# Performance work log

Measured on AMD Instinct MI355X. Metric: run time of the kernel, lower is better.

Reference implementation:

```python
import jax, jax.numpy as jnp
import numpy as np

HIST_SIZE = 200
DIM = 64
HIDDEN = 32
NEG_INF = -2.0**32 + 1.0  # matches tf padding constant


def setup_inputs() -> dict:
    key = jax.random.key(0)
    k1, k2, k3, k4, k5 = jax.random.split(key, 5)
    B = 4096
    cand = jax.random.normal(k1, (B, DIM), dtype=jnp.float32)
    hist = jax.random.normal(k2, (B, HIST_SIZE, DIM), dtype=jnp.float32)
    hisLens = jax.random.randint(k3, (B,), 0, HIST_SIZE, dtype=jnp.int32)
    # Glorot-normal-ish params
    attW1 = jax.random.normal(k4, (4 * DIM, HIDDEN), dtype=jnp.float32) * (2.0 / (4 * DIM + HIDDEN)) ** 0.5
    attB1 = jnp.zeros((HIDDEN,), dtype=jnp.float32)
    attW2 = jax.random.normal(k5, (HIDDEN, 1), dtype=jnp.float32) * (2.0 / (HIDDEN + 1)) ** 0.5
    attB2 = jnp.zeros((1,), dtype=jnp.float32)
    return {"candidate_embedding": cand, "hist_embeddings": hist, "hisLens": hisLens,
            "attW1": attW1, "attB1": attB1, "attW2": attW2, "attB2": attB2}


def reference(candidate_embedding, hist_embeddings, hisLens, attW1, attB1, attW2, attB2):
    # candidate: [B, d] -> broadcast over hist steps [B, S, d]
    cand = candidate_embedding[:, None, :]
    # per-step feature concat: [cand, hist, cand*hist, cand-hist] -> [B, S, 4d]
    z3 = jnp.concatenate([
        jnp.broadcast_to(cand, hist_embeddings.shape),
        hist_embeddings,
        cand * hist_embeddings,
        cand - hist_embeddings,
    ], axis=-1)
    # tiny 2-layer MLP scorer -> [B, S]
    h = jax.nn.relu(jnp.einsum('bsf,fh->bsh', z3, attW1) + attB1)
    scores = (jnp.einsum('bsh,ho->bso', h, attW2) + attB2)[..., 0]
    # sequence mask then scale (same order as original), softmax over hist dim
    mask = jnp.arange(HIST_SIZE)[None, :] < hisLens[:, None]
    scores = jnp.where(mask, scores, NEG_INF) / (DIM ** 0.5)
    w = jax.nn.softmax(scores, axis=-1)  # [B, S]
    # weighted sum of history embeddings -> [B, d]
    return jnp.einsum('bs,bsd->bd', w, hist_embeddings)
```

## Files before the change

kernel.cpp:

```cpp
#include <hip/hip_runtime.h>
#include <math.h>

#define HS    200
#define DIMV  64
#define HID   32
#define NTH   256
#define NB    2

typedef __attribute__((ext_vector_type(8))) short short8;
typedef __attribute__((ext_vector_type(4))) float f32x4;
typedef __bf16 bf2_t __attribute__((ext_vector_type(2)));
typedef float  f2_t  __attribute__((ext_vector_type(2)));

__device__ __forceinline__ unsigned cvt2(float x, float y) {
    f2_t f = {x, y};
    bf2_t bv = __builtin_convertvector(f, bf2_t);
    union { bf2_t b; unsigned u; } un;
    un.b = bv;
    return un.u;
}

template<int CTRL>
__device__ __forceinline__ float dpp_add(float x) {
    int y = __builtin_amdgcn_update_dpp(0, __float_as_int(x), CTRL, 0xF, 0xF, true);
    return x + __int_as_float(y);
}
#define ROR1  0x121
#define ROR2  0x122
#define ROR4  0x124
#define ROR8  0x128
#define QXOR1 0xB1
#define QXOR2 0x4E
#define HMIRR 0x141
__device__ __forceinline__ float swz_xor16(float x) {
    return __int_as_float(__builtin_amdgcn_ds_swizzle(__float_as_int(x), 0x401F));
}
__device__ __forceinline__ float rfl(float x) {
    return __int_as_float(__builtin_amdgcn_readfirstlane(__float_as_int(x)));
}


__global__ __launch_bounds__(NTH, 4) void din_attn_kernel(
    const float* __restrict__ cand,
    const float* __restrict__ hist,
    const int*   __restrict__ lens,
    const float* __restrict__ W1,
    const float* __restrict__ B1,
    const float* __restrict__ W2,
    const float* __restrict__ B2,
    float* __restrict__ out)
{
    __shared__ __align__(16) unsigned short s_Mt[NB][HID * 64];
    __shared__ float s_c[NB][HID];
    __shared__ __align__(16) float s_comb[4][DIMV];
    __shared__ float s_m[4], s_l[4];

    const int tid  = threadIdx.x;
    const int lane = tid & 63, wid = tid >> 6;
    const int b0   = blockIdx.x * NB;

    {
        const int h = tid & 31, fg = tid >> 5;
        float wbd[8], wcc[8];
        #pragma unroll
        for (int ff = 0; ff < 8; ++ff) {
            int f = fg * 8 + ff;
            wbd[ff] = W1[(DIMV + f) * HID + h] - W1[(3 * DIMV + f) * HID + h];
            wcc[ff] = W1[(2 * DIMV + f) * HID + h];
        }
        #pragma unroll
        for (int k = 0; k < NB; ++k) {
            const float* cb = cand + (size_t)(b0 + k) * DIMV + fg * 8;
            float4 cA = *(const float4*)cb;
            float4 cB = *(const float4*)(cb + 4);
            float cf[8] = {cA.x, cA.y, cA.z, cA.w, cB.x, cB.y, cB.z, cB.w};
            float m[8];
            #pragma unroll
            for (int ff = 0; ff < 8; ++ff) m[ff] = fmaf(cf[ff], wcc[ff], wbd[ff]);
            uint4 mw = make_uint4(cvt2(m[0], m[1]), cvt2(m[2], m[3]),
                                  cvt2(m[4], m[5]), cvt2(m[6], m[7]));
            *(uint4*)&s_Mt[k][h * 64 + (fg ^ (h & 7)) * 8] = mw;
        }
        const int hc = tid >> 3, fgc = tid & 7;
        float wad[8];
        #pragma unroll
        for (int ff = 0; ff < 8; ++ff) {
            int f = fgc * 8 + ff;
            wad[ff] = W1[f * HID + hc] + W1[(3 * DIMV + f) * HID + hc];
        }
        float b1 = B1[hc];
        #pragma unroll
        for (int k = 0; k < NB; ++k) {
            const float* cb = cand + (size_t)(b0 + k) * DIMV + fgc * 8;
            float4 cA = *(const float4*)cb;
            float4 cB = *(const float4*)(cb + 4);
            float p = cA.x * wad[0] + cA.y * wad[1] + cA.z * wad[2] + cA.w * wad[3]
                    + cB.x * wad[4] + cB.y * wad[5] + cB.z * wad[6] + cB.w * wad[7];
            p = dpp_add<QXOR1>(p);
            p = dpp_add<QXOR2>(p);
            p = dpp_add<HMIRR>(p);
            if ((tid & 7) == 0) s_c[k][hc] = p + b1;
        }
    }
    __syncthreads();

    const int kb   = wid >> 1, hf = wid & 1;
    const int b    = b0 + kb;
    const int len  = lens[b];
    const bool uni = (len == 0);
    const int nrow  = uni ? HS : len;
    const int nhalf = (nrow + 1 - hf) >> 1;
    const int nt    = (nhalf + 15) >> 4;
    const int lc    = lane & 15, lg = lane >> 4;
    const float* hb = hist + (size_t)b * (HS * DIMV);

    short8 b00 = *(const short8*)&s_Mt[kb][lc * 64        + ((lg)     ^ (lc & 7)) * 8];
    short8 b01 = *(const short8*)&s_Mt[kb][lc * 64        + ((4 + lg) ^ (lc & 7)) * 8];
    short8 b10 = *(const short8*)&s_Mt[kb][(16 + lc) * 64 + ((lg)     ^ (lc & 7)) * 8];
    short8 b11 = *(const short8*)&s_Mt[kb][(16 + lc) * 64 + ((4 + lg) ^ (lc & 7)) * 8];
    const float c0  = s_c[kb][lc],     c1  = s_c[kb][16 + lc];
    const float w20 = W2[lc] * 0.125f, w21 = W2[16 + lc] * 0.125f;

    float m_run = -3.0e38f, l_acc = 0.f;
    float o0[8] = {0.f, 0.f, 0.f, 0.f, 0.f, 0.f, 0.f, 0.f};
    float o1[8] = {0.f, 0.f, 0.f, 0.f, 0.f, 0.f, 0.f, 0.f};

    for (int rt = 0; rt < nt; ++rt) {
        int i = rt * 16 + lc;
        if (i > nhalf - 1) i = nhalf - 1;
        const int s = 2 * i + hf;
        const float* ap = hb + s * 64 + lg * 8;
        float4 A00 = *(const float4*)ap;
        float4 A01 = *(const float4*)(ap + 4);
        float4 A10 = *(const float4*)(ap + 32);
        float4 A11 = *(const float4*)(ap + 36);
        union { uint4 u; short8 s8; } u0, u1;
        u0.u = make_uint4(cvt2(A00.x, A00.y), cvt2(A00.z, A00.w),
                          cvt2(A01.x, A01.y), cvt2(A01.z, A01.w));
        u1.u = make_uint4(cvt2(A10.x, A10.y), cvt2(A10.z, A10.w),
                          cvt2(A11.x, A11.y), cvt2(A11.z, A11.w));

        f32x4 acc0 = {c0, c0, c0, c0};
        acc0 = __builtin_amdgcn_mfma_f32_16x16x32_bf16(u0.s8, b00, acc0, 0, 0, 0);
        acc0 = __builtin_amdgcn_mfma_f32_16x16x32_bf16(u1.s8, b01, acc0, 0, 0, 0);
        f32x4 acc1 = {c1, c1, c1, c1};
        acc1 = __builtin_amdgcn_mfma_f32_16x16x32_bf16(u0.s8, b10, acc1, 0, 0, 0);
        acc1 = __builtin_amdgcn_mfma_f32_16x16x32_bf16(u1.s8, b11, acc1, 0, 0, 0);

        float p[4];
        #pragma unroll
        for (int r = 0; r < 4; ++r)
            p[r] = fmaxf(acc0[r], 0.f) * w20 + fmaxf(acc1[r], 0.f) * w21;
        #pragma unroll
        for (int r = 0; r < 4; ++r) {
            p[r] = dpp_add<ROR1>(p[r]);
            p[r] = dpp_add<ROR2>(p[r]);
            p[r] = dpp_add<ROR4>(p[r]);
            p[r] = dpp_add<ROR8>(p[r]);
        }
        #pragma unroll
        for (int r = 0; r < 4; ++r) {
            int row = rt * 16 + lg * 4 + r;
            p[r] = (row < nhalf) ? (uni ? 0.f : p[r]) : -4.0e9f;
        }
        float tmax = fmaxf(fmaxf(p[0], p[1]), fmaxf(p[2], p[3]));
        tmax = fmaxf(tmax, swz_xor16(tmax));
        tmax = fmaxf(tmax, __shfl_xor(tmax, 32));
        tmax = rfl(tmax);
        if (tmax > m_run + 8.f) {
            float sf = __expf(m_run - tmax);
            #pragma unroll
            for (int j = 0; j < 8; ++j) { o0[j] *= sf; o1[j] *= sf; }
            l_acc *= sf;
            m_run = tmax;
        }
        float e[4];
        #pragma unroll
        for (int r = 0; r < 4; ++r) e[r] = __expf(p[r] - m_run);
        l_acc += (e[0] + e[1]) + (e[2] + e[3]);

        float t0 = (lc & 1) ? e[1] : e[0];
        float t1 = (lc & 1) ? e[3] : e[2];
        float es = (lc & 2) ? t1 : t0;
        int   src = (((lc & 3) | ((lc >> 2) << 4)) << 2);
        float wrow = __int_as_float(
            __builtin_amdgcn_ds_bpermute(src, __float_as_int(es)));

        o0[0] = fmaf(wrow, A00.x, o0[0]); o0[1] = fmaf(wrow, A00.y, o0[1]);
        o0[2] = fmaf(wrow, A00.z, o0[2]); o0[3] = fmaf(wrow, A00.w, o0[3]);
        o0[4] = fmaf(wrow, A01.x, o0[4]); o0[5] = fmaf(wrow, A01.y, o0[5]);
        o0[6] = fmaf(wrow, A01.z, o0[6]); o0[7] = fmaf(wrow, A01.w, o0[7]);
        o1[0] = fmaf(wrow, A10.x, o1[0]); o1[1] = fmaf(wrow, A10.y, o1[1]);
        o1[2] = fmaf(wrow, A10.z, o1[2]); o1[3] = fmaf(wrow, A10.w, o1[3]);
        o1[4] = fmaf(wrow, A11.x, o1[4]); o1[5] = fmaf(wrow, A11.y, o1[5]);
        o1[6] = fmaf(wrow, A11.z, o1[6]); o1[7] = fmaf(wrow, A11.w, o1[7]);
    }

    l_acc += swz_xor16(l_acc);
    l_acc += __shfl_xor(l_acc, 32);
    #pragma unroll
    for (int j = 0; j < 8; ++j) {
        float x = o0[j];
        x = dpp_add<ROR1>(x); x = dpp_add<ROR2>(x);
        x = dpp_add<ROR4>(x); x = dpp_add<ROR8>(x);
        o0[j] = x;
        float y = o1[j];
        y = dpp_add<ROR1>(y); y = dpp_add<ROR2>(y);
        y = dpp_add<ROR4>(y); y = dpp_add<ROR8>(y);
        o1[j] = y;
    }
    if (lc == 0) {
        float* d = &s_comb[wid][lg * 8];
        *(float4*)d        = make_float4(o0[0], o0[1], o0[2], o0[3]);
        *(float4*)(d + 4)  = make_float4(o0[4], o0[5], o0[6], o0[7]);
        *(float4*)(d + 32) = make_float4(o1[0], o1[1], o1[2], o1[3]);
        *(float4*)(d + 36) = make_float4(o1[4], o1[5], o1[6], o1[7]);
        if (lane == 0) { s_m[wid] = m_run; s_l[wid] = l_acc; }
    }
    __syncthreads();

    if (wid < NB) {
        const int w0 = 2 * wid, w1 = 2 * wid + 1;
        const float m0 = s_m[w0], m1 = s_m[w1];
        const float M  = fmaxf(m0, m1);
        const float a0 = __expf(m0 - M), a1 = __expf(m1 - M);
        const float den = a0 * s_l[w0] + a1 * s_l[w1];
        const float o   = a0 * s_comb[w0][lane] + a1 * s_comb[w1][lane];
        out[(size_t)(b0 + wid) * DIMV + lane] = o / den;
    }
}

extern "C" void kernel_launch(void* const* d_in, const int* in_sizes, int n_in,
                              void* d_out, int out_size, void* d_ws, size_t ws_size,
                              hipStream_t stream) {
    const float* cand = (const float*)d_in[0];
    const float* hist = (const float*)d_in[1];
    const int*   lens = (const int*)d_in[2];
    const float* W1   = (const float*)d_in[3];
    const float* B1   = (const float*)d_in[4];
    const float* W2   = (const float*)d_in[5];
    const float* B2   = (const float*)d_in[6];
    float* out = (float*)d_out;

    const int B = in_sizes[0] / DIMV;
    const int GRID = B / NB;
    din_attn_kernel<<<GRID, NTH, 0, stream>>>(cand, hist, lens, W1, B1, W2, B2, out);
}
```

Baseline: 35.34 us.

## Balance history tiles across waves with an LDS work counter over four batches

```diff
diff --git a/kernel.cpp b/kernel.cpp
--- a/kernel.cpp
+++ b/kernel.cpp
@@ -5,7 +5,7 @@
 #define DIMV  64
 #define HID   32
 #define NTH   256
-#define NB    2
+#define NB    4
 
 typedef __attribute__((ext_vector_type(8))) short short8;
 typedef __attribute__((ext_vector_type(4))) float f32x4;
@@ -19,6 +19,8 @@
     un.b = bv;
     return un.u;
 }
+__device__ __forceinline__ float blo(unsigned u) { return __uint_as_float(u << 16); }
+__device__ __forceinline__ float bhi(unsigned u) { return __uint_as_float(u & 0xFFFF0000u); }
 
 template<int CTRL>
 __device__ __forceinline__ float dpp_add(float x) {
@@ -52,8 +54,9 @@
 {
     __shared__ __align__(16) unsigned short s_Mt[NB][HID * 64];
     __shared__ float s_c[NB][HID];
-    __shared__ __align__(16) float s_comb[4][DIMV];
-    __shared__ float s_m[4], s_l[4];
+    __shared__ __align__(16) float s_om[4][NB][DIMV];
+    __shared__ float s_mm[4][NB], s_ll[4][NB];
+    __shared__ int   s_ctr;
 
     const int tid  = threadIdx.x;
     const int lane = tid & 63, wid = tid >> 6;
@@ -101,35 +104,78 @@
             p = dpp_add<HMIRR>(p);
             if ((tid & 7) == 0) s_c[k][hc] = p + b1;
         }
+        if (tid < 16) { s_mm[tid >> 2][tid & 3] = -3.0e38f; s_ll[tid >> 2][tid & 3] = 0.f; }
+        if (tid == 0) s_ctr = 0;
     }
     __syncthreads();
 
-    const int kb   = wid >> 1, hf = wid & 1;
-    const int b    = b0 + kb;
-    const int len  = lens[b];
-    const bool uni = (len == 0);
-    const int nrow  = uni ? HS : len;
-    const int nhalf = (nrow + 1 - hf) >> 1;
-    const int nt    = (nhalf + 15) >> 4;
-    const int lc    = lane & 15, lg = lane >> 4;
-    const float* hb = hist + (size_t)b * (HS * DIMV);
-
-    short8 b00 = *(const short8*)&s_Mt[kb][lc * 64        + ((lg)     ^ (lc & 7)) * 8];
-    short8 b01 = *(const short8*)&s_Mt[kb][lc * 64        + ((4 + lg) ^ (lc & 7)) * 8];
-    short8 b10 = *(const short8*)&s_Mt[kb][(16 + lc) * 64 + ((lg)     ^ (lc & 7)) * 8];
-    short8 b11 = *(const short8*)&s_Mt[kb][(16 + lc) * 64 + ((4 + lg) ^ (lc & 7)) * 8];
-    const float c0  = s_c[kb][lc],     c1  = s_c[kb][16 + lc];
+    const int lc = lane & 15, lg = lane >> 4;
     const float w20 = W2[lc] * 0.125f, w21 = W2[16 + lc] * 0.125f;
-
+    const int len0 = lens[b0 + 0], len1 = lens[b0 + 1];
+    const int len2 = lens[b0 + 2], len3 = lens[b0 + 3];
+    const int nr0 = (len0 == 0) ? HS : len0, nr1 = (len1 == 0) ? HS : len1;
+    const int nr2 = (len2 == 0) ? HS : len2, nr3 = (len3 == 0) ? HS : len3;
+    const int t0 = (nr0 + 15) >> 4, t1 = (nr1 + 15) >> 4;
+    const int t2 = (nr2 + 15) >> 4, t3 = (nr3 + 15) >> 4;
+    const int q1 = t0, q2 = t0 + t1, q3 = t0 + t1 + t2;
+    const int total = q3 + t3;
+
+    int curk = -1, nrow = 0;
+    bool uni = false;
+    float c0 = 0.f, c1 = 0.f;
     float m_run = -3.0e38f, l_acc = 0.f;
     float o0[8] = {0.f, 0.f, 0.f, 0.f, 0.f, 0.f, 0.f, 0.f};
     float o1[8] = {0.f, 0.f, 0.f, 0.f, 0.f, 0.f, 0.f, 0.f};
-
-    for (int rt = 0; rt < nt; ++rt) {
+    const float* hb = hist;
+
+    auto FLUSH = [&](int kk) {
+        float l = l_acc;
+        l += swz_xor16(l);
+        l += __shfl_xor(l, 32);
+        #pragma unroll
+        for (int jj = 0; jj < 8; ++jj) {
+            float x = o0[jj];
+            x = dpp_add<ROR1>(x); x = dpp_add<ROR2>(x);
+            x = dpp_add<ROR4>(x); x = dpp_add<ROR8>(x);
+            o0[jj] = x;
+            float y = o1[jj];
+            y = dpp_add<ROR1>(y); y = dpp_add<ROR2>(y);
+            y = dpp_add<ROR4>(y); y = dpp_add<ROR8>(y);
+            o1[jj] = y;
+        }
+        if (lc == 0) {
+            float* d = &s_om[wid][kk][lg * 8];
+            *(float4*)d        = make_float4(o0[0], o0[1], o0[2], o0[3]);
+            *(float4*)(d + 4)  = make_float4(o0[4], o0[5], o0[6], o0[7]);
+            *(float4*)(d + 32) = make_float4(o1[0], o1[1], o1[2], o1[3]);
+            *(float4*)(d + 36) = make_float4(o1[4], o1[5], o1[6], o1[7]);
+            if (lane == 0) { s_mm[wid][kk] = m_run; s_ll[wid][kk] = l; }
+        }
+    };
+
+    for (;;) {
+        int j = 0;
+        if (lane == 0) j = atomicAdd(&s_ctr, 1);
+        j = __shfl(j, 0);
+        if (j >= total) break;
+        const int k  = (j >= q1) + (j >= q2) + (j >= q3);
+        const int rt = j - ((k == 0) ? 0 : (k == 1) ? q1 : (k == 2) ? q2 : q3);
+        if (k != curk) {
+            if (curk >= 0) FLUSH(curk);
+            curk = k;
+            m_run = -3.0e38f; l_acc = 0.f;
+            #pragma unroll
+            for (int jj = 0; jj < 8; ++jj) { o0[jj] = 0.f; o1[jj] = 0.f; }
+            c0 = s_c[k][lc]; c1 = s_c[k][16 + lc];
+            const int lk = (k == 0) ? len0 : (k == 1) ? len1 : (k == 2) ? len2 : len3;
+            uni  = (lk == 0);
+            nrow = (k == 0) ? nr0 : (k == 1) ? nr1 : (k == 2) ? nr2 : nr3;
+            hb   = hist + (size_t)(b0 + k) * (HS * DIMV);
+        }
+
         int i = rt * 16 + lc;
-        if (i > nhalf - 1) i = nhalf - 1;
-        const int s = 2 * i + hf;
-        const float* ap = hb + s * 64 + lg * 8;
+        if (i > nrow - 1) i = nrow - 1;
+        const float* ap = hb + i * 64 + lg * 8;
         float4 A00 = *(const float4*)ap;
         float4 A01 = *(const float4*)(ap + 4);
         float4 A10 = *(const float4*)(ap + 32);
@@ -140,6 +186,12 @@
         u1.u = make_uint4(cvt2(A10.x, A10.y), cvt2(A10.z, A10.w),
                           cvt2(A11.x, A11.y), cvt2(A11.z, A11.w));
 
+        const unsigned short* mt = s_Mt[k];
+        short8 b00 = *(const short8*)&mt[lc * 64        + ((lg)     ^ (lc & 7)) * 8];
+        short8 b01 = *(const short8*)&mt[lc * 64        + ((4 + lg) ^ (lc & 7)) * 8];
+        short8 b10 = *(const short8*)&mt[(16 + lc) * 64 + ((lg)     ^ (lc & 7)) * 8];
+        short8 b11 = *(const short8*)&mt[(16 + lc) * 64 + ((4 + lg) ^ (lc & 7)) * 8];
+
         f32x4 acc0 = {c0, c0, c0, c0};
         acc0 = __builtin_amdgcn_mfma_f32_16x16x32_bf16(u0.s8, b00, acc0, 0, 0, 0);
         acc0 = __builtin_amdgcn_mfma_f32_16x16x32_bf16(u1.s8, b01, acc0, 0, 0, 0);
@@ -161,7 +213,7 @@
         #pragma unroll
         for (int r = 0; r < 4; ++r) {
             int row = rt * 16 + lg * 4 + r;
-            p[r] = (row < nhalf) ? (uni ? 0.f : p[r]) : -4.0e9f;
+            p[r] = (row < nrow) ? (uni ? 0.f : p[r]) : -4.0e9f;
         }
         float tmax = fmaxf(fmaxf(p[0], p[1]), fmaxf(p[2], p[3]));
         tmax = fmaxf(tmax, swz_xor16(tmax));
@@ -170,7 +222,7 @@
         if (tmax > m_run + 8.f) {
             float sf = __expf(m_run - tmax);
             #pragma unroll
-            for (int j = 0; j < 8; ++j) { o0[j] *= sf; o1[j] *= sf; }
+            for (int jj = 0; jj < 8; ++jj) { o0[jj] *= sf; o1[jj] *= sf; }
             l_acc *= sf;
             m_run = tmax;
         }
@@ -179,53 +231,35 @@
         for (int r = 0; r < 4; ++r) e[r] = __expf(p[r] - m_run);
         l_acc += (e[0] + e[1]) + (e[2] + e[3]);
 
-        float t0 = (lc & 1) ? e[1] : e[0];
-        float t1 = (lc & 1) ? e[3] : e[2];
-        float es = (lc & 2) ? t1 : t0;
+        float s0 = (lc & 1) ? e[1] : e[0];
+        float s1 = (lc & 1) ? e[3] : e[2];
+        float es = (lc & 2) ? s1 : s0;
         int   src = (((lc & 3) | ((lc >> 2) << 4)) << 2);
         float wrow = __int_as_float(
             __builtin_amdgcn_ds_bpermute(src, __float_as_int(es)));
 
-        o0[0] = fmaf(wrow, A00.x, o0[0]); o0[1] = fmaf(wrow, A00.y, o0[1]);
-        o0[2] = fmaf(wrow, A00.z, o0[2]); o0[3] = fmaf(wrow, A00.w, o0[3]);
-        o0[4] = fmaf(wrow, A01.x, o0[4]); o0[5] = fmaf(wrow, A01.y, o0[5]);
-        o0[6] = fmaf(wrow, A01.z, o0[6]); o0[7] = fmaf(wrow, A01.w, o0[7]);
-        o1[0] = fmaf(wrow, A10.x, o1[0]); o1[1] = fmaf(wrow, A10.y, o1[1]);
-        o1[2] = fmaf(wrow, A10.z, o1[2]); o1[3] = fmaf(wrow, A10.w, o1[3]);
-        o1[4] = fmaf(wrow, A11.x, o1[4]); o1[5] = fmaf(wrow, A11.y, o1[5]);
-        o1[6] = fmaf(wrow, A11.z, o1[6]); o1[7] = fmaf(wrow, A11.w, o1[7]);
+        o0[0] = fmaf(wrow, blo(u0.u.x), o0[0]); o0[1] = fmaf(wrow, bhi(u0.u.x), o0[1]);
+        o0[2] = fmaf(wrow, blo(u0.u.y), o0[2]); o0[3] = fmaf(wrow, bhi(u0.u.y), o0[3]);
+        o0[4] = fmaf(wrow, blo(u0.u.z), o0[4]); o0[5] = fmaf(wrow, bhi(u0.u.z), o0[5]);
+        o0[6] = fmaf(wrow, blo(u0.u.w), o0[6]); o0[7] = fmaf(wrow, bhi(u0.u.w), o0[7]);
+        o1[0] = fmaf(wrow, blo(u1.u.x), o1[0]); o1[1] = fmaf(wrow, bhi(u1.u.x), o1[1]);
+        o1[2] = fmaf(wrow, blo(u1.u.y), o1[2]); o1[3] = fmaf(wrow, bhi(u1.u.y), o1[3]);
+        o1[4] = fmaf(wrow, blo(u1.u.z), o1[4]); o1[5] = fmaf(wrow, bhi(u1.u.z), o1[5]);
+        o1[6] = fmaf(wrow, blo(u1.u.w), o1[6]); o1[7] = fmaf(wrow, bhi(u1.u.w), o1[7]);
     }
-
-    l_acc += swz_xor16(l_acc);
-    l_acc += __shfl_xor(l_acc, 32);
-    #pragma unroll
-    for (int j = 0; j < 8; ++j) {
-        float x = o0[j];
-        x = dpp_add<ROR1>(x); x = dpp_add<ROR2>(x);
-        x = dpp_add<ROR4>(x); x = dpp_add<ROR8>(x);
-        o0[j] = x;
-        float y = o1[j];
-        y = dpp_add<ROR1>(y); y = dpp_add<ROR2>(y);
-        y = dpp_add<ROR4>(y); y = dpp_add<ROR8>(y);
-        o1[j] = y;
-    }
-    if (lc == 0) {
-        float* d = &s_comb[wid][lg * 8];
-        *(float4*)d        = make_float4(o0[0], o0[1], o0[2], o0[3]);
-        *(float4*)(d + 4)  = make_float4(o0[4], o0[5], o0[6], o0[7]);
-        *(float4*)(d + 32) = make_float4(o1[0], o1[1], o1[2], o1[3]);
-        *(float4*)(d + 36) = make_float4(o1[4], o1[5], o1[6], o1[7]);
-        if (lane == 0) { s_m[wid] = m_run; s_l[wid] = l_acc; }
-    }
+    if (curk >= 0) FLUSH(curk);
     __syncthreads();
 
-    if (wid < NB) {
-        const int w0 = 2 * wid, w1 = 2 * wid + 1;
-        const float m0 = s_m[w0], m1 = s_m[w1];
-        const float M  = fmaxf(m0, m1);
+    {
+        const float m0 = s_mm[0][wid], m1 = s_mm[1][wid];
+        const float m2 = s_mm[2][wid], m3 = s_mm[3][wid];
+        const float M  = fmaxf(fmaxf(m0, m1), fmaxf(m2, m3));
         const float a0 = __expf(m0 - M), a1 = __expf(m1 - M);
-        const float den = a0 * s_l[w0] + a1 * s_l[w1];
-        const float o   = a0 * s_comb[w0][lane] + a1 * s_comb[w1][lane];
+        const float a2 = __expf(m2 - M), a3 = __expf(m3 - M);
+        const float den = a0 * s_ll[0][wid] + a1 * s_ll[1][wid]
+                        + a2 * s_ll[2][wid] + a3 * s_ll[3][wid];
+        const float o = a0 * s_om[0][wid][lane] + a1 * s_om[1][wid][lane]
+                      + a2 * s_om[2][wid][lane] + a3 * s_om[3][wid][lane];
         out[(size_t)(b0 + wid) * DIMV + lane] = o / den;
     }
 }
```

Result: faster. 32.99 us (-6.6%).

## Raise occupancy by cutting registers: reload B fragments from LDS, reuse bf16 history

Applied to the files above, without the earlier changes.

```diff
diff --git a/kernel.cpp b/kernel.cpp
--- a/kernel.cpp
+++ b/kernel.cpp
@@ -19,6 +19,8 @@
     un.b = bv;
     return un.u;
 }
+__device__ __forceinline__ float blo(unsigned u) { return __uint_as_float(u << 16); }
+__device__ __forceinline__ float bhi(unsigned u) { return __uint_as_float(u & 0xFFFF0000u); }
 
 template<int CTRL>
 __device__ __forceinline__ float dpp_add(float x) {
@@ -40,7 +42,7 @@
 }
 
 
-__global__ __launch_bounds__(NTH, 4) void din_attn_kernel(
+__global__ __launch_bounds__(NTH, 8) void din_attn_kernel(
     const float* __restrict__ cand,
     const float* __restrict__ hist,
     const int*   __restrict__ lens,
@@ -113,11 +115,8 @@
     const int nt    = (nhalf + 15) >> 4;
     const int lc    = lane & 15, lg = lane >> 4;
     const float* hb = hist + (size_t)b * (HS * DIMV);
-
-    short8 b00 = *(const short8*)&s_Mt[kb][lc * 64        + ((lg)     ^ (lc & 7)) * 8];
-    short8 b01 = *(const short8*)&s_Mt[kb][lc * 64        + ((4 + lg) ^ (lc & 7)) * 8];
-    short8 b10 = *(const short8*)&s_Mt[kb][(16 + lc) * 64 + ((lg)     ^ (lc & 7)) * 8];
-    short8 b11 = *(const short8*)&s_Mt[kb][(16 + lc) * 64 + ((4 + lg) ^ (lc & 7)) * 8];
+    const unsigned short* mt = s_Mt[kb];
+
     const float c0  = s_c[kb][lc],     c1  = s_c[kb][16 + lc];
     const float w20 = W2[lc] * 0.125f, w21 = W2[16 + lc] * 0.125f;
 
@@ -141,11 +140,15 @@
                           cvt2(A11.x, A11.y), cvt2(A11.z, A11.w));
 
         f32x4 acc0 = {c0, c0, c0, c0};
-        acc0 = __builtin_amdgcn_mfma_f32_16x16x32_bf16(u0.s8, b00, acc0, 0, 0, 0);
-        acc0 = __builtin_amdgcn_mfma_f32_16x16x32_bf16(u1.s8, b01, acc0, 0, 0, 0);
+        acc0 = __builtin_amdgcn_mfma_f32_16x16x32_bf16(u0.s8,
+            *(const short8*)&mt[lc * 64        + ((lg)     ^ (lc & 7)) * 8], acc0, 0, 0, 0);
+        acc0 = __builtin_amdgcn_mfma_f32_16x16x32_bf16(u1.s8,
+            *(const short8*)&mt[lc * 64        + ((4 + lg) ^ (lc & 7)) * 8], acc0, 0, 0, 0);
         f32x4 acc1 = {c1, c1, c1, c1};
-        acc1 = __builtin_amdgcn_mfma_f32_16x16x32_bf16(u0.s8, b10, acc1, 0, 0, 0);
-        acc1 = __builtin_amdgcn_mfma_f32_16x16x32_bf16(u1.s8, b11, acc1, 0, 0, 0);
+        acc1 = __builtin_amdgcn_mfma_f32_16x16x32_bf16(u0.s8,
+            *(const short8*)&mt[(16 + lc) * 64 + ((lg)     ^ (lc & 7)) * 8], acc1, 0, 0, 0);
+        acc1 = __builtin_amdgcn_mfma_f32_16x16x32_bf16(u1.s8,
+            *(const short8*)&mt[(16 + lc) * 64 + ((4 + lg) ^ (lc & 7)) * 8], acc1, 0, 0, 0);
 
         float p[4];
         #pragma unroll
@@ -186,14 +189,14 @@
         float wrow = __int_as_float(
             __builtin_amdgcn_ds_bpermute(src, __float_as_int(es)));
 
-        o0[0] = fmaf(wrow, A00.x, o0[0]); o0[1] = fmaf(wrow, A00.y, o0[1]);
-        o0[2] = fmaf(wrow, A00.z, o0[2]); o0[3] = fmaf(wrow, A00.w, o0[3]);
-        o0[4] = fmaf(wrow, A01.x, o0[4]); o0[5] = fmaf(wrow, A01.y, o0[5]);
-        o0[6] = fmaf(wrow, A01.z, o0[6]); o0[7] = fmaf(wrow, A01.w, o0[7]);
-        o1[0] = fmaf(wrow, A10.x, o1[0]); o1[1] = fmaf(wrow, A10.y, o1[1]);
-        o1[2] = fmaf(wrow, A10.z, o1[2]); o1[3] = fmaf(wrow, A10.w, o1[3]);
-        o1[4] = fmaf(wrow, A11.x, o1[4]); o1[5] = fmaf(wrow, A11.y, o1[5]);
-        o1[6] = fmaf(wrow, A11.z, o1[6]); o1[7] = fmaf(wrow, A11.w, o1[7]);
+        o0[0] = fmaf(wrow, blo(u0.u.x), o0[0]); o0[1] = fmaf(wrow, bhi(u0.u.x), o0[1]);
+        o0[2] = fmaf(wrow, blo(u0.u.y), o0[2]); o0[3] = fmaf(wrow, bhi(u0.u.y), o0[3]);
+        o0[4] = fmaf(wrow, blo(u0.u.z), o0[4]); o0[5] = fmaf(wrow, bhi(u0.u.z), o0[5]);
+        o0[6] = fmaf(wrow, blo(u0.u.w), o0[6]); o0[7] = fmaf(wrow, bhi(u0.u.w), o0[7]);
+        o1[0] = fmaf(wrow, blo(u1.u.x), o1[0]); o1[1] = fmaf(wrow, bhi(u1.u.x), o1[1]);
+        o1[2] = fmaf(wrow, blo(u1.u.y), o1[2]); o1[3] = fmaf(wrow, bhi(u1.u.y), o1[3]);
+        o1[4] = fmaf(wrow, blo(u1.u.z), o1[4]); o1[5] = fmaf(wrow, bhi(u1.u.z), o1[5]);
+        o1[6] = fmaf(wrow, blo(u1.u.w), o1[6]); o1[7] = fmaf(wrow, bhi(u1.u.w), o1[7]);
     }
 
     l_acc += swz_xor16(l_acc);
```

Measured after the change: 47.80 us. +35.3%, slower.
